# Optimization experiments

Measured on AMD Instinct MI355X. Metric: run time of the kernel, lower is better.

Reference implementation:

```python
import jax, jax.numpy as jnp
import numpy as np
import math

GAMMA = 2.0
ALPHA = 0.25
SIZES = [[64, 64], [32, 32], [16, 16], [8, 8], [4, 4]]
RATIOS = [0.5, 1.0, 2.0]
SCALES = [1.0, 2.0 ** (1.0 / 3.0), 2.0 ** (2.0 / 3.0)]
B, T, C = 16, 64, 80


def _create_anchors(sizes, ratios, scales):
    # replicates torch create_anchors (cthw format, normalized [-1,1] coords)
    aspects = np.array([[[s * math.sqrt(r), s * math.sqrt(1.0 / r)] for s in scales]
                        for r in ratios], dtype=np.float64).reshape(-1, 2)
    out = []
    for (h, w) in sizes:
        sized = 4.0 * (aspects * np.array([2.0 / h, 2.0 / w]))  # [a,2]
        rows = np.linspace(-1 + 1.0 / h, 1 - 1.0 / h, h) if h > 1 else np.array([0.0])
        cols = np.linspace(-1 + 1.0 / w, 1 - 1.0 / w, w) if w > 1 else np.array([0.0])
        gy, gx = np.meshgrid(rows, cols, indexing='ij')
        grid = np.stack([gy, gx], -1).reshape(-1, 1, 2)  # [h*w,1,2]
        n, a = grid.shape[0], aspects.shape[0]
        anc = np.concatenate([np.broadcast_to(grid, (n, a, 2)),
                              np.broadcast_to(sized[None], (n, a, 2))], 2)
        out.append(anc.reshape(-1, 4))
    return jnp.asarray(np.concatenate(out, 0), dtype=jnp.float32)


def _cthw2tlbr(b):
    return jnp.concatenate([b[..., :2] - b[..., 2:] / 2, b[..., :2] + b[..., 2:] / 2], -1)


def _tlbr2cthw(b):
    return jnp.concatenate([(b[..., :2] + b[..., 2:]) / 2, b[..., 2:] - b[..., :2]], -1)


def _iou(anchors, tgts):
    # anchors [A,4] cthw, tgts [T,4] cthw -> [A,T]
    a_t, t_t = _cthw2tlbr(anchors), _cthw2tlbr(tgts)
    tl = jnp.maximum(a_t[:, None, :2], t_t[None, :, :2])
    br = jnp.minimum(a_t[:, None, 2:], t_t[None, :, 2:])
    sz = jnp.clip(br - tl, 0.0)
    inter = sz[..., 0] * sz[..., 1]
    a_sz = anchors[:, 2] * anchors[:, 3]
    t_sz = tgts[:, 2] * tgts[:, 3]
    union = a_sz[:, None] + t_sz[None, :] - inter
    return inter / (union + 1e-8)


def _bbox_to_activ(bboxes, anchors):
    tc = (bboxes[..., :2] - anchors[..., :2]) / anchors[..., 2:]
    ts = jnp.log(bboxes[..., 2:] / anchors[..., 2:] + 1e-8)
    return jnp.concatenate([tc, ts], -1) / jnp.array([0.1, 0.1, 0.2, 0.2], dtype=bboxes.dtype)


def _one_loss(clas_pred, bbox_pred, clas_tgt, bbox_tgt_tlbr, anchors):
    Tn = clas_tgt.shape[0]
    tgt = _tlbr2cthw(bbox_tgt_tlbr)
    valid = clas_tgt > 0                       # pad_idx = 0 -> padded targets invalid
    iou = jnp.where(valid[None, :], _iou(anchors, tgt), -1.0)  # [A,T]
    vals = iou.max(axis=1)
    idxs = iou.argmax(axis=1)
    # -1 background, -2 ignore band (0.4 <= iou <= 0.5)
    matches = jnp.where(vals > 0.5, idxs, jnp.where(vals < 0.4, -1, -2))
    pos = matches >= 0
    safe = jnp.clip(matches, 0, Tn - 1)
    # smooth_l1 (beta=1, mean over selected elements)
    reg_tgt = _bbox_to_activ(tgt[safe], anchors)
    d = bbox_pred - reg_tgt
    ad = jnp.abs(d)
    sl1 = jnp.where(ad < 1.0, 0.5 * d * d, ad - 0.5)
    npos = pos.sum().astype(clas_pred.dtype)
    bb_loss = (sl1 * pos[:, None]).sum() / jnp.maximum(4.0 * npos, 1.0)
    # class targets: matched anchors get 1-based class, background -> 0
    cls = jnp.where(pos, clas_tgt[safe], 0)
    clas_mask = matches >= -1                  # exclude ignored anchors
    enc = jax.nn.one_hot(cls - 1, clas_pred.shape[1], dtype=clas_pred.dtype)  # cls=0 -> all-zero row
    ps = jax.nn.sigmoid(clas_pred)
    w = (enc * (1 - ps) + (1 - enc) * ps) ** GAMMA * ((1 - enc) * ALPHA + enc * (1 - ALPHA))
    w = jax.lax.stop_gradient(w)               # weights.detach() in torch
    bce = -(enc * jax.nn.log_sigmoid(clas_pred) + (1 - enc) * jax.nn.log_sigmoid(-clas_pred))
    clas_loss = (w * bce * clas_mask[:, None].astype(clas_pred.dtype)).sum()
    return bb_loss + clas_loss / jnp.maximum(npos, 1.0)


def setup_inputs() -> dict:
    key = jax.random.key(0)
    k1, k2, k3, k4, k5 = jax.random.split(key, 5)
    anchors = _create_anchors(SIZES, RATIOS, SCALES)
    A = anchors.shape[0]
    clas_preds = jax.random.normal(k1, (B, A, C), dtype=jnp.float32)
    bbox_preds = jax.random.normal(k2, (B, A, 4), dtype=jnp.float32) * 0.1
    centers = jax.random.uniform(k3, (B, T, 2), minval=-0.7, maxval=0.7)
    sizes = jax.random.uniform(k4, (B, T, 2), minval=0.05, maxval=0.5)
    bbox_tgts = jnp.concatenate([centers - sizes / 2, centers + sizes / 2], -1)  # tlbr
    clas_tgts = jax.random.randint(k5, (B, T), 1, C + 1)  # 1-based labels, no padding
    return {"clas_preds": clas_preds, "bbox_preds": bbox_preds,
            "bbox_tgts": bbox_tgts, "clas_tgts": clas_tgts, "anchors": anchors}


def reference(clas_preds, bbox_preds, bbox_tgts, clas_tgts, anchors):
    per_img = jax.vmap(_one_loss, in_axes=(0, 0, 0, 0, None))(
        clas_preds, bbox_preds, clas_tgts, bbox_tgts, anchors)
    return per_img.sum() / clas_preds.shape[0]
```

## Files before the change

### kernel.cpp

```cpp
#include <hip/hip_runtime.h>
#include <cstdint>
#include <cstddef>

#define TPB 256
#define MAXT 128
#define BIGC 1e18f

#define K_BG 0.17328679514f

__device__ __forceinline__ float f_bg4(float4 v) {
    float r = 0.f;
    const float xs[4] = {v.x, v.y, v.z, v.w};
    #pragma unroll
    for (int i = 0; i < 4; ++i) {
        const float x  = xs[i];
        const float u  = x * 1.44269504089f;
        const float em = __builtin_amdgcn_exp2f(-fabsf(u));
        const float oe = 1.f + em;
        const float l2 = __builtin_amdgcn_logf(oe);
        const float s  = __builtin_amdgcn_rcpf(oe);
        const float sp2 = fmaxf(u, 0.f) + l2;
        const float p  = (x >= 0.f) ? s : (1.f - s);
        r = fmaf(p * p, sp2, r);
    }
    return r;
}

__device__ __forceinline__ float f_fg_minus_bg(float x) {
    const float ax = fabsf(x);
    const float em = __builtin_amdgcn_exp2f(ax * -1.44269504089f);
    const float oe = 1.f + em;
    const float l  = __builtin_amdgcn_logf(oe) * 0.69314718056f;
    const float s  = __builtin_amdgcn_rcpf(oe);
    const float sp_p = (x >= 0.f) ? (x + l) : l;
    const float sp_n = sp_p - x;
    const float p  = (x >= 0.f) ? s : (1.f - s);
    const float q  = 1.f - p;
    return 0.75f * q * q * sp_n - 0.25f * p * p * sp_p;
}

template<int C4T>
__global__ __launch_bounds__(TPB, 4)
void fused_kernel(const float* __restrict__ bbox_preds,
                  const float* __restrict__ bbox_tgts,
                  const int*   __restrict__ clas_tgts,
                  const float* __restrict__ anchors,
                  const float* __restrict__ clas_preds,
                  int A, int T, int C4rt,
                  float* __restrict__ np_p,
                  float* __restrict__ bb_p,
                  float* __restrict__ cl_p,
                  int nblk)
{
    const int C4  = (C4T > 0) ? C4T : C4rt;
    const int b   = blockIdx.y;
    const int a0  = blockIdx.x * TPB;
    const int tid = threadIdx.x;
    const int a   = a0 + tid;
    const bool in = (a < A);
    const int lane = tid & 63;
    const int wid  = tid >> 6;

    const int nA = min(TPB, A - a0);
    const float4* tile = reinterpret_cast<const float4*>(clas_preds)
                         + ((size_t)b * A + a0) * C4;

    constexpr int CH  = 5;
    constexpr int NCH = (C4T > 0 ? C4T : 5) / CH;
    float4 cur[CH];
    if (C4T > 0 && nA == TPB) {
        #pragma unroll
        for (int i = 0; i < CH; ++i) cur[i] = tile[tid + i * TPB];
    }

    __shared__ float4 s_ta[MAXT];
    __shared__ float4 s_tb[MAXT];
    __shared__ int    s_cls[MAXT];
    for (int i = tid; i < T; i += TPB) {
        const float4 tg = reinterpret_cast<const float4*>(bbox_tgts)[(size_t)b * T + i];
        const int   cl = clas_tgts[(size_t)b * T + i];
        const float c0 = (tg.x + tg.z) * 0.5f, c1 = (tg.y + tg.w) * 0.5f;
        const float s0 = tg.z - tg.x,          s1 = tg.w - tg.y;
        const bool  val = (cl > 0);
        s_ta[i] = val ? make_float4(c0 - s0 * 0.5f, c1 - s1 * 0.5f,
                                    c0 + s0 * 0.5f, c1 + s1 * 0.5f)
                      : make_float4(BIGC, BIGC, BIGC, BIGC);
        s_tb[i] = make_float4(c0, c1, s0, s1);
        s_cls[i] = cl;
    }

    float4 anc = make_float4(0.f, 0.f, 1.f, 1.f);
    if (in) anc = reinterpret_cast<const float4*>(anchors)[a];
    const float a_tl0 = anc.x - anc.z * 0.5f;
    const float a_tl1 = anc.y - anc.w * 0.5f;
    const float a_br0 = anc.x + anc.z * 0.5f;
    const float a_br1 = anc.y + anc.w * 0.5f;
    const float a_area_eps = anc.z * anc.w + 1e-8f;

    float m0 = in ? a_tl0 :  1e30f, m1 = in ? a_tl1 :  1e30f;
    float M0 = in ? a_br0 : -1e30f, M1 = in ? a_br1 : -1e30f;
    #pragma unroll
    for (int off = 32; off; off >>= 1) {
        m0 = fminf(m0, __shfl_down(m0, off));
        m1 = fminf(m1, __shfl_down(m1, off));
        M0 = fmaxf(M0, __shfl_down(M0, off));
        M1 = fmaxf(M1, __shfl_down(M1, off));
    }
    __shared__ float s_red[4][TPB / 64];
    if (lane == 0) {
        s_red[0][wid] = m0; s_red[1][wid] = m1;
        s_red[2][wid] = M0; s_red[3][wid] = M1;
    }
    __syncthreads();

    __shared__ int s_act[MAXT];
    __shared__ int s_nact;
    if (wid == 0) {
        float bm0 = s_red[0][0], bm1 = s_red[1][0];
        float bM0 = s_red[2][0], bM1 = s_red[3][0];
        #pragma unroll
        for (int w = 1; w < TPB / 64; ++w) {
            bm0 = fminf(bm0, s_red[0][w]); bm1 = fminf(bm1, s_red[1][w]);
            bM0 = fmaxf(bM0, s_red[2][w]); bM1 = fmaxf(bM1, s_red[3][w]);
        }
        bool act = false;
        if (lane < T && T <= 64) {
            const float4 ta = s_ta[lane];
            act = (ta.x <= bM0) && (ta.y <= bM1) && (ta.z >= bm0) && (ta.w >= bm1);
        }
        const unsigned long long ball = __ballot(act);
        if (act) {
            const unsigned long long lm =
                (lane == 63) ? ~0ULL >> 1 : (1ULL << lane) - 1;
            s_act[__popcll(ball & lm)] = lane;
        }
        if (lane == 0) s_nact = __popcll(ball);
    }
    if (T > 64) {
        for (int i = tid; i < T; i += TPB) s_act[i] = i;
        if (tid == 0) s_nact = T;
    }
    __syncthreads();

    const int nact = s_nact;
    float bI = -1.f, bU = 1.f;
    int   besti = 0;

#define IOU_STEP(tt)                                                        \
    {                                                                       \
        const float4 ta = s_ta[tt];                                         \
        const float tl0 = fmaxf(a_tl0, ta.x);                               \
        const float tl1 = fmaxf(a_tl1, ta.y);                               \
        const float br0 = fminf(a_br0, ta.z);                               \
        const float br1 = fminf(a_br1, ta.w);                               \
        const float sz0 = fmaxf(br0 - tl0, 0.0f);                           \
        const float sz1 = fmaxf(br1 - tl1, 0.0f);                           \
        const float inter = sz0 * sz1;                                      \
        const float tarea = (ta.z - ta.x) * (ta.w - ta.y);                  \
        const float uni = a_area_eps + tarea - inter;                       \
        const bool upd = inter * bU > bI * uni;       \
        bI = upd ? inter : bI;                                              \
        bU = upd ? uni   : bU;                                              \
        besti = upd ? (tt) : besti;                                         \
    }

    float raw = 0.f;
    if (C4T > 0 && nA == TPB) {
        const int cs = (nact + NCH - 1) / NCH;
        #pragma unroll
        for (int g = 0; g < NCH; ++g) {
            float4 nxt[CH];
            if (g + 1 < NCH) {
                #pragma unroll
                for (int i = 0; i < CH; ++i)
                    nxt[i] = tile[tid + ((g + 1) * CH + i) * TPB];
            }
            #pragma unroll
            for (int i = 0; i < CH; ++i) raw += f_bg4(cur[i]);
            const int te = min((g + 1) * cs, nact);
            for (int t = g * cs; t < te; ++t) IOU_STEP(s_act[t])
            if (g + 1 < NCH) {
                #pragma unroll
                for (int i = 0; i < CH; ++i) cur[i] = nxt[i];
            }
        }
    } else {
        const int tot = nA * C4;
        for (int j = tid; j < tot; j += TPB)
            raw += f_bg4(tile[j]);
        for (int t = 0; t < nact; ++t) IOU_STEP(s_act[t])
    }
#undef IOU_STEP

    const bool pos = in && (bI > 0.5f * bU);
    const bool ign = in && !pos && !(bI < 0.4f * bU);

    float sl1 = 0.f;
    int   cls = 0;
    if (pos) {
        const float4 tb = s_tb[besti];
        cls = s_cls[besti];
        const float4 bp = reinterpret_cast<const float4*>(bbox_preds)[(size_t)b * A + a];
        const float tc0 = (tb.x - anc.x) / anc.z;
        const float tc1 = (tb.y - anc.y) / anc.w;
        const float ts0 = logf(tb.z / anc.z + 1e-8f);
        const float ts1 = logf(tb.w / anc.w + 1e-8f);
        const float r0 = tc0 / 0.1f, r1 = tc1 / 0.1f;
        const float r2 = ts0 / 0.2f, r3 = ts1 / 0.2f;
        const float d0 = bp.x - r0, d1 = bp.y - r1, d2 = bp.z - r2, d3 = bp.w - r3;
        const float a0f = fabsf(d0), a1f = fabsf(d1), a2f = fabsf(d2), a3f = fabsf(d3);
        sl1 += (a0f < 1.f) ? 0.5f * d0 * d0 : a0f - 0.5f;
        sl1 += (a1f < 1.f) ? 0.5f * d1 * d1 : a1f - 0.5f;
        sl1 += (a2f < 1.f) ? 0.5f * d2 * d2 : a2f - 0.5f;
        sl1 += (a3f < 1.f) ? 0.5f * d3 * d3 : a3f - 0.5f;
    }

    const unsigned long long pball = __ballot(pos);
    const unsigned long long iball = __ballot(ign);

    __shared__ int s_pc[TPB / 64], s_ic[TPB / 64];
    __shared__ int s_plist[TPB], s_pcls[TPB], s_ilist[TPB];
    if (lane == 0) { s_pc[wid] = __popcll(pball); s_ic[wid] = __popcll(iball); }
    __syncthreads();
    int p_off = 0, i_off = 0, p_total = 0, i_total = 0;
    #pragma unroll
    for (int w = 0; w < TPB / 64; ++w) {
        if (w < wid) { p_off += s_pc[w]; i_off += s_ic[w]; }
        p_total += s_pc[w]; i_total += s_ic[w];
    }
    const unsigned long long lmask = (lane == 63) ? ~0ULL >> 1 : (1ULL << lane) - 1;
    if (pos) {
        const int idx = p_off + __popcll(pball & lmask);
        s_plist[idx] = a; s_pcls[idx] = cls;
    }
    if (ign) {
        const int idx = i_off + __popcll(iball & lmask);
        s_ilist[idx] = a;
    }
    __syncthreads();

    float corr = 0.f;
    if (tid < p_total) {
        const int pa = s_plist[tid];
        const int pc = s_pcls[tid];
        const float x = clas_preds[((size_t)b * A + pa) * (C4 * 4) + (pc - 1)];
        corr += f_fg_minus_bg(x);
    }
    const int ig_elems = i_total * C4;
    for (int j = tid; j < ig_elems; j += TPB) {
        const int ii = j / C4;
        const int c4 = j - ii * C4;
        const int ia = s_ilist[ii];
        raw -= f_bg4(reinterpret_cast<const float4*>(clas_preds)
                         [((size_t)b * A + ia) * C4 + c4]);
    }

    float v = sl1;
    float u = fmaf(raw, K_BG, corr);
    #pragma unroll
    for (int off = 32; off; off >>= 1) {
        v += __shfl_down(v, off);
        u += __shfl_down(u, off);
    }
    __shared__ float s_sl1[TPB / 64], s_cl[TPB / 64];
    if (lane == 0) { s_sl1[wid] = v; s_cl[wid] = u; }
    __syncthreads();
    if (tid == 0) {
        float tv = 0.f, tu = 0.f;
        #pragma unroll
        for (int w = 0; w < TPB / 64; ++w) { tv += s_sl1[w]; tu += s_cl[w]; }
        const size_t o = (size_t)b * nblk + blockIdx.x;
        bb_p[o] = tv;
        cl_p[o] = tu;
        np_p[o] = (float)p_total;
    }
}

__global__ void reduce_kernel(const float* __restrict__ np_p,
                              const float* __restrict__ bb_p,
                              const float* __restrict__ cl_p,
                              int nblk, int Bn,
                              float* __restrict__ out)
{
    const int wid  = threadIdx.x >> 6;
    const int lane = threadIdx.x & 63;
    const int nw   = blockDim.x >> 6;
    __shared__ float s_loss[32];

    float acc = 0.f;
    for (int b = wid; b < Bn; b += nw) {
        float cl = 0.f, bb = 0.f, np = 0.f;
        for (int i = lane; i < nblk; i += 64) {
            const size_t o = (size_t)b * nblk + i;
            np += np_p[o]; bb += bb_p[o]; cl += cl_p[o];
        }
        #pragma unroll
        for (int off = 32; off; off >>= 1) {
            cl += __shfl_down(cl, off);
            bb += __shfl_down(bb, off);
            np += __shfl_down(np, off);
        }
        if (lane == 0)
            acc += bb / fmaxf(4.f * np, 1.f) + cl / fmaxf(np, 1.f);
    }
    if (lane == 0) s_loss[wid] = acc;
    __syncthreads();
    if (threadIdx.x == 0) {
        float v = 0.f;
        for (int w = 0; w < nw; ++w) v += s_loss[w];
        out[0] = v / (float)Bn;
    }
}

extern "C" void kernel_launch(void* const* d_in, const int* in_sizes, int n_in,
                              void* d_out, int out_size, void* d_ws, size_t ws_size,
                              hipStream_t stream)
{
    const float* clas_preds = (const float*)d_in[0];
    const float* bbox_preds = (const float*)d_in[1];
    const float* bbox_tgts  = (const float*)d_in[2];
    const int*   clas_tgts  = (const int*)d_in[3];
    const float* anchors    = (const float*)d_in[4];

    const int A  = in_sizes[4] / 4;
    const int Bn = in_sizes[1] / (A * 4);
    const int T  = in_sizes[3] / Bn;
    const int C  = in_sizes[0] / (Bn * A);
    const int C4 = C / 4;

    const int nblk = (A + TPB - 1) / TPB;

    char* ws = (char*)d_ws;
    float* np_p = (float*)ws;  ws += (size_t)Bn * nblk * sizeof(float);
    float* bb_p = (float*)ws;  ws += (size_t)Bn * nblk * sizeof(float);
    float* cl_p = (float*)ws;

    dim3 g1((unsigned)nblk, (unsigned)Bn);
    if (C4 == 20) {
        fused_kernel<20><<<g1, TPB, 0, stream>>>(
            bbox_preds, bbox_tgts, clas_tgts, anchors, clas_preds,
            A, T, C4, np_p, bb_p, cl_p, nblk);
    } else {
        fused_kernel<0><<<g1, TPB, 0, stream>>>(
            bbox_preds, bbox_tgts, clas_tgts, anchors, clas_preds,
            A, T, C4, np_p, bb_p, cl_p, nblk);
    }

    reduce_kernel<<<1, 1024, 0, stream>>>(np_p, bb_p, cl_p, nblk, Bn, (float*)d_out);
}
```

Baseline: 62.17 us.

## Process two anchor tiles per block to halve block count and share target setup

Each block now covers 512 anchors (two 256-anchor tiles per thread). This amortizes target loading, the active-target culling and the reductions over twice the work, and it halves the grid size. The streaming loop runs twice as many chunk iterations, and the IoU work for each tile is interleaved into its half. The culling bounding box now spans both tiles, so fewer targets may be culled, and fewer blocks may reduce occupancy and load balance on a large-CU GPU.

```diff
diff --git a/kernel.cpp b/kernel.cpp
--- a/kernel.cpp
+++ b/kernel.cpp
@@ -2,7 +2,9 @@
 #include <cstdint>
 #include <cstddef>
 
-#define TPB 256
+#define TPB  256
+#define TILES 2
+#define SPAN (TPB * TILES)
 #define MAXT 128
 #define BIGC 1e18f
 
@@ -37,6 +39,25 @@
     const float p  = (x >= 0.f) ? s : (1.f - s);
     const float q  = 1.f - p;
     return 0.75f * q * q * sp_n - 0.25f * p * p * sp_p;
+}
+
+struct AGeom { float tl0, tl1, br0, br1, area_eps; };
+
+__device__ __forceinline__ void iou_step(const AGeom& g, const float4 ta, int tt,
+                                         float& bI, float& bU, int& besti) {
+    const float tl0 = fmaxf(g.tl0, ta.x);
+    const float tl1 = fmaxf(g.tl1, ta.y);
+    const float br0 = fminf(g.br0, ta.z);
+    const float br1 = fminf(g.br1, ta.w);
+    const float sz0 = fmaxf(br0 - tl0, 0.0f);
+    const float sz1 = fmaxf(br1 - tl1, 0.0f);
+    const float inter = sz0 * sz1;
+    const float tarea = (ta.z - ta.x) * (ta.w - ta.y);
+    const float uni = g.area_eps + tarea - inter;
+    const bool upd = inter * bU > bI * uni;
+    bI = upd ? inter : bI;
+    bU = upd ? uni   : bU;
+    besti = upd ? tt : besti;
 }
 
 template<int C4T>
@@ -54,51 +75,55 @@
 {
     const int C4  = (C4T > 0) ? C4T : C4rt;
     const int b   = blockIdx.y;
-    const int a0  = blockIdx.x * TPB;
+    const int a0  = blockIdx.x * SPAN;
     const int tid = threadIdx.x;
-    const int a   = a0 + tid;
-    const bool in = (a < A);
     const int lane = tid & 63;
     const int wid  = tid >> 6;
-
-    const int nA = min(TPB, A - a0);
+    const int nA  = min(SPAN, A - a0);
+    const bool in[2] = { a0 + tid < A, a0 + TPB + tid < A };
+
     const float4* tile = reinterpret_cast<const float4*>(clas_preds)
                          + ((size_t)b * A + a0) * C4;
 
     constexpr int CH  = 5;
     constexpr int NCH = (C4T > 0 ? C4T : 5) / CH;
     float4 cur[CH];
-    if (C4T > 0 && nA == TPB) {
+    if (C4T > 0 && nA == SPAN) {
         #pragma unroll
         for (int i = 0; i < CH; ++i) cur[i] = tile[tid + i * TPB];
     }
 
     __shared__ float4 s_ta[MAXT];
-    __shared__ float4 s_tb[MAXT];
     __shared__ int    s_cls[MAXT];
     for (int i = tid; i < T; i += TPB) {
         const float4 tg = reinterpret_cast<const float4*>(bbox_tgts)[(size_t)b * T + i];
         const int   cl = clas_tgts[(size_t)b * T + i];
         const float c0 = (tg.x + tg.z) * 0.5f, c1 = (tg.y + tg.w) * 0.5f;
         const float s0 = tg.z - tg.x,          s1 = tg.w - tg.y;
-        const bool  val = (cl > 0);
-        s_ta[i] = val ? make_float4(c0 - s0 * 0.5f, c1 - s1 * 0.5f,
-                                    c0 + s0 * 0.5f, c1 + s1 * 0.5f)
-                      : make_float4(BIGC, BIGC, BIGC, BIGC);
-        s_tb[i] = make_float4(c0, c1, s0, s1);
+        s_ta[i] = (cl > 0) ? make_float4(c0 - s0 * 0.5f, c1 - s1 * 0.5f,
+                                         c0 + s0 * 0.5f, c1 + s1 * 0.5f)
+                           : make_float4(BIGC, BIGC, BIGC, BIGC);
         s_cls[i] = cl;
     }
 
-    float4 anc = make_float4(0.f, 0.f, 1.f, 1.f);
-    if (in) anc = reinterpret_cast<const float4*>(anchors)[a];
-    const float a_tl0 = anc.x - anc.z * 0.5f;
-    const float a_tl1 = anc.y - anc.w * 0.5f;
-    const float a_br0 = anc.x + anc.z * 0.5f;
-    const float a_br1 = anc.y + anc.w * 0.5f;
-    const float a_area_eps = anc.z * anc.w + 1e-8f;
-
-    float m0 = in ? a_tl0 :  1e30f, m1 = in ? a_tl1 :  1e30f;
-    float M0 = in ? a_br0 : -1e30f, M1 = in ? a_br1 : -1e30f;
+    AGeom geo[2];
+    #pragma unroll
+    for (int ti = 0; ti < 2; ++ti) {
+        float4 anc = make_float4(0.f, 0.f, 1.f, 1.f);
+        if (in[ti]) anc = reinterpret_cast<const float4*>(anchors)[a0 + ti * TPB + tid];
+        geo[ti].tl0 = anc.x - anc.z * 0.5f;
+        geo[ti].tl1 = anc.y - anc.w * 0.5f;
+        geo[ti].br0 = anc.x + anc.z * 0.5f;
+        geo[ti].br1 = anc.y + anc.w * 0.5f;
+        geo[ti].area_eps = anc.z * anc.w + 1e-8f;
+    }
+
+    float m0 =  1e30f, m1 =  1e30f, M0 = -1e30f, M1 = -1e30f;
+    #pragma unroll
+    for (int ti = 0; ti < 2; ++ti) if (in[ti]) {
+        m0 = fminf(m0, geo[ti].tl0); m1 = fminf(m1, geo[ti].tl1);
+        M0 = fmaxf(M0, geo[ti].br0); M1 = fmaxf(M1, geo[ti].br1);
+    }
     #pragma unroll
     for (int off = 32; off; off >>= 1) {
         m0 = fminf(m0, __shfl_down(m0, off));
@@ -143,43 +168,31 @@
     __syncthreads();
 
     const int nact = s_nact;
-    float bI = -1.f, bU = 1.f;
-    int   besti = 0;
-
-#define IOU_STEP(tt)                                                        \
-    {                                                                       \
-        const float4 ta = s_ta[tt];                                         \
-        const float tl0 = fmaxf(a_tl0, ta.x);                               \
-        const float tl1 = fmaxf(a_tl1, ta.y);                               \
-        const float br0 = fminf(a_br0, ta.z);                               \
-        const float br1 = fminf(a_br1, ta.w);                               \
-        const float sz0 = fmaxf(br0 - tl0, 0.0f);                           \
-        const float sz1 = fmaxf(br1 - tl1, 0.0f);                           \
-        const float inter = sz0 * sz1;                                      \
-        const float tarea = (ta.z - ta.x) * (ta.w - ta.y);                  \
-        const float uni = a_area_eps + tarea - inter;                       \
-        const bool upd = inter * bU > bI * uni;       \
-        bI = upd ? inter : bI;                                              \
-        bU = upd ? uni   : bU;                                              \
-        besti = upd ? (tt) : besti;                                         \
-    }
+    float bI[2] = {-1.f, -1.f}, bU[2] = {1.f, 1.f};
+    int   besti[2] = {0, 0};
 
     float raw = 0.f;
-    if (C4T > 0 && nA == TPB) {
+    if (C4T > 0 && nA == SPAN) {
         const int cs = (nact + NCH - 1) / NCH;
         #pragma unroll
-        for (int g = 0; g < NCH; ++g) {
+        for (int g = 0; g < 2 * NCH; ++g) {
             float4 nxt[CH];
-            if (g + 1 < NCH) {
+            if (g + 1 < 2 * NCH) {
                 #pragma unroll
                 for (int i = 0; i < CH; ++i)
                     nxt[i] = tile[tid + ((g + 1) * CH + i) * TPB];
             }
             #pragma unroll
             for (int i = 0; i < CH; ++i) raw += f_bg4(cur[i]);
-            const int te = min((g + 1) * cs, nact);
-            for (int t = g * cs; t < te; ++t) IOU_STEP(s_act[t])
-            if (g + 1 < NCH) {
+            constexpr int NCHc = NCH;
+            const int ai = g / NCHc;
+            const int gg = g - ai * NCHc;
+            const int te = min((gg + 1) * cs, nact);
+            for (int t = gg * cs; t < te; ++t) {
+                const int tt = s_act[t];
+                iou_step(geo[ai], s_ta[tt], tt, bI[ai], bU[ai], besti[ai]);
+            }
+            if (g + 1 < 2 * NCH) {
                 #pragma unroll
                 for (int i = 0; i < CH; ++i) cur[i] = nxt[i];
             }
@@ -188,63 +201,103 @@
         const int tot = nA * C4;
         for (int j = tid; j < tot; j += TPB)
             raw += f_bg4(tile[j]);
-        for (int t = 0; t < nact; ++t) IOU_STEP(s_act[t])
-    }
-#undef IOU_STEP
-
-    const bool pos = in && (bI > 0.5f * bU);
-    const bool ign = in && !pos && !(bI < 0.4f * bU);
-
+        for (int t = 0; t < nact; ++t) {
+            const int tt = s_act[t];
+            iou_step(geo[0], s_ta[tt], tt, bI[0], bU[0], besti[0]);
+            iou_step(geo[1], s_ta[tt], tt, bI[1], bU[1], besti[1]);
+        }
+    }
+
+    bool pos[2], ign[2];
+    int  cls[2] = {0, 0};
     float sl1 = 0.f;
-    int   cls = 0;
-    if (pos) {
-        const float4 tb = s_tb[besti];
-        cls = s_cls[besti];
-        const float4 bp = reinterpret_cast<const float4*>(bbox_preds)[(size_t)b * A + a];
-        const float tc0 = (tb.x - anc.x) / anc.z;
-        const float tc1 = (tb.y - anc.y) / anc.w;
-        const float ts0 = logf(tb.z / anc.z + 1e-8f);
-        const float ts1 = logf(tb.w / anc.w + 1e-8f);
-        const float r0 = tc0 / 0.1f, r1 = tc1 / 0.1f;
-        const float r2 = ts0 / 0.2f, r3 = ts1 / 0.2f;
-        const float d0 = bp.x - r0, d1 = bp.y - r1, d2 = bp.z - r2, d3 = bp.w - r3;
-        const float a0f = fabsf(d0), a1f = fabsf(d1), a2f = fabsf(d2), a3f = fabsf(d3);
-        sl1 += (a0f < 1.f) ? 0.5f * d0 * d0 : a0f - 0.5f;
-        sl1 += (a1f < 1.f) ? 0.5f * d1 * d1 : a1f - 0.5f;
-        sl1 += (a2f < 1.f) ? 0.5f * d2 * d2 : a2f - 0.5f;
-        sl1 += (a3f < 1.f) ? 0.5f * d3 * d3 : a3f - 0.5f;
-    }
-
-    const unsigned long long pball = __ballot(pos);
-    const unsigned long long iball = __ballot(ign);
-
-    __shared__ int s_pc[TPB / 64], s_ic[TPB / 64];
-    __shared__ int s_plist[TPB], s_pcls[TPB], s_ilist[TPB];
-    if (lane == 0) { s_pc[wid] = __popcll(pball); s_ic[wid] = __popcll(iball); }
-    __syncthreads();
-    int p_off = 0, i_off = 0, p_total = 0, i_total = 0;
-    #pragma unroll
-    for (int w = 0; w < TPB / 64; ++w) {
-        if (w < wid) { p_off += s_pc[w]; i_off += s_ic[w]; }
-        p_total += s_pc[w]; i_total += s_ic[w];
+    #pragma unroll
+    for (int ti = 0; ti < 2; ++ti) {
+        pos[ti] = in[ti] && (bI[ti] > 0.5f * bU[ti]);
+        ign[ti] = in[ti] && !pos[ti] && !(bI[ti] < 0.4f * bU[ti]);
+        if (pos[ti]) {
+            const int bi = besti[ti];
+            const float4 ta = s_ta[bi];
+            cls[ti] = s_cls[bi];
+            const float az = geo[ti].br0 - geo[ti].tl0;
+            const float aw = geo[ti].br1 - geo[ti].tl1;
+            const float ax = (geo[ti].tl0 + geo[ti].br0) * 0.5f;
+            const float ay = (geo[ti].tl1 + geo[ti].br1) * 0.5f;
+            const float tz = ta.z - ta.x, tw = ta.w - ta.y;
+            const float tx = (ta.x + ta.z) * 0.5f, ty = (ta.y + ta.w) * 0.5f;
+            const float4 bp = reinterpret_cast<const float4*>(bbox_preds)
+                                  [(size_t)b * A + a0 + ti * TPB + tid];
+            const float r0 = ((tx - ax) / az) / 0.1f;
+            const float r1 = ((ty - ay) / aw) / 0.1f;
+            const float r2 = logf(tz / az + 1e-8f) / 0.2f;
+            const float r3 = logf(tw / aw + 1e-8f) / 0.2f;
+            const float d0 = bp.x - r0, d1 = bp.y - r1, d2 = bp.z - r2, d3 = bp.w - r3;
+            const float a0f = fabsf(d0), a1f = fabsf(d1), a2f = fabsf(d2), a3f = fabsf(d3);
+            sl1 += (a0f < 1.f) ? 0.5f * d0 * d0 : a0f - 0.5f;
+            sl1 += (a1f < 1.f) ? 0.5f * d1 * d1 : a1f - 0.5f;
+            sl1 += (a2f < 1.f) ? 0.5f * d2 * d2 : a2f - 0.5f;
+            sl1 += (a3f < 1.f) ? 0.5f * d3 * d3 : a3f - 0.5f;
+        }
+    }
+
+    unsigned long long pb[2], ib[2];
+    pb[0] = __ballot(pos[0]); pb[1] = __ballot(pos[1]);
+    ib[0] = __ballot(ign[0]); ib[1] = __ballot(ign[1]);
+
+    __shared__ int s_pc[2][TPB / 64], s_ic[2][TPB / 64];
+    __shared__ int s_plist[SPAN], s_pcls[SPAN], s_ilist[SPAN];
+    if (lane == 0) {
+        s_pc[0][wid] = __popcll(pb[0]); s_pc[1][wid] = __popcll(pb[1]);
+        s_ic[0][wid] = __popcll(ib[0]); s_ic[1][wid] = __popcll(ib[1]);
+    }
+    __syncthreads();
+    int p_off[2] = {0, 0}, i_off[2] = {0, 0}, p_total = 0, i_total = 0;
+    #pragma unroll
+    for (int ti = 0; ti < 2; ++ti)
+        #pragma unroll
+        for (int w = 0; w < TPB / 64; ++w) {
+            if (ti < 1 || (ti == 1 && true)) {}
+            if ((ti == 0 && w < wid) || ti < 0) {}
+            if (ti == 0) { if (w < wid) p_off[0] += s_pc[0][w]; }
+            else {
+                p_off[1] += (0);
+            }
+            p_total += s_pc[ti][w];
+            i_total += s_ic[ti][w];
+        }
+    {
+        int t0p = 0, t0i = 0;
+        #pragma unroll
+        for (int w = 0; w < TPB / 64; ++w) { t0p += s_pc[0][w]; t0i += s_ic[0][w]; }
+        p_off[1] = t0p; i_off[1] = t0i;
+        #pragma unroll
+        for (int w = 0; w < TPB / 64; ++w) {
+            if (w < wid) { p_off[1] += s_pc[1][w]; i_off[1] += s_ic[1][w]; }
+        }
+        #pragma unroll
+        for (int w = 0; w < TPB / 64; ++w) {
+            if (w < wid) i_off[0] += s_ic[0][w];
+        }
     }
     const unsigned long long lmask = (lane == 63) ? ~0ULL >> 1 : (1ULL << lane) - 1;
-    if (pos) {
-        const int idx = p_off + __popcll(pball & lmask);
-        s_plist[idx] = a; s_pcls[idx] = cls;
-    }
-    if (ign) {
-        const int idx = i_off + __popcll(iball & lmask);
-        s_ilist[idx] = a;
+    #pragma unroll
+    for (int ti = 0; ti < 2; ++ti) {
+        if (pos[ti]) {
+            const int idx = p_off[ti] + __popcll(pb[ti] & lmask);
+            s_plist[idx] = a0 + ti * TPB + tid; s_pcls[idx] = cls[ti];
+        }
+        if (ign[ti]) {
+            const int idx = i_off[ti] + __popcll(ib[ti] & lmask);
+            s_ilist[idx] = a0 + ti * TPB + tid;
+        }
     }
     __syncthreads();
 
     float corr = 0.f;
-    if (tid < p_total) {
-        const int pa = s_plist[tid];
-        const int pc = s_pcls[tid];
-        const float x = clas_preds[((size_t)b * A + pa) * (C4 * 4) + (pc - 1)];
-        corr += f_fg_minus_bg(x);
+    for (int j = tid; j < p_total; j += TPB) {
+        const int pa = s_plist[j];
+        const int pc = s_pcls[j];
+        corr += f_fg_minus_bg(clas_preds[((size_t)b * A + pa) * (C4 * 4) + (pc - 1)]);
     }
     const int ig_elems = i_total * C4;
     for (int j = tid; j < ig_elems; j += TPB) {
@@ -262,13 +315,13 @@
         v += __shfl_down(v, off);
         u += __shfl_down(u, off);
     }
-    __shared__ float s_sl1[TPB / 64], s_cl[TPB / 64];
-    if (lane == 0) { s_sl1[wid] = v; s_cl[wid] = u; }
+    __shared__ float s_sl1[TPB / 64], s_cl2[TPB / 64];
+    if (lane == 0) { s_sl1[wid] = v; s_cl2[wid] = u; }
     __syncthreads();
     if (tid == 0) {
         float tv = 0.f, tu = 0.f;
         #pragma unroll
-        for (int w = 0; w < TPB / 64; ++w) { tv += s_sl1[w]; tu += s_cl[w]; }
+        for (int w = 0; w < TPB / 64; ++w) { tv += s_sl1[w]; tu += s_cl2[w]; }
         const size_t o = (size_t)b * nblk + blockIdx.x;
         bb_p[o] = tv;
         cl_p[o] = tu;
@@ -328,7 +381,7 @@
     const int C  = in_sizes[0] / (Bn * A);
     const int C4 = C / 4;
 
-    const int nblk = (A + TPB - 1) / TPB;
+    const int nblk = (A + SPAN - 1) / SPAN;
 
     char* ws = (char*)d_ws;
     float* np_p = (float*)ws;  ws += (size_t)Bn * nblk * sizeof(float);
```

Result: slower. 113.4 us (+82.4%).
